# Kernel optimization log

Hardware: AMD Instinct MI355X
Metric: run time of the kernel (lower is better)

## Reference

```python
import jax, jax.numpy as jnp
import numpy as np

FORE_TH = 0.5
BACK_TH = 0.4
MAX_FOR_TARGET = True
FOREGROUND_ONLY = False  # return both foreground and background masks


def _cxcywh_to_xyxy(b):
    cx, cy, w, h = b[..., 0], b[..., 1], b[..., 2], b[..., 3]
    return jnp.stack([cx - w * 0.5, cy - h * 0.5, cx + w * 0.5, cy + h * 0.5], axis=-1)


def _batch_iou(anchors_xyxy, boxes_xyxy):
    # anchors_xyxy: [A,4], boxes_xyxy: [B,T,4] -> ious [B,A,T]
    a = anchors_xyxy[None, :, None, :]   # [1,A,1,4]
    b = boxes_xyxy[:, None, :, :]        # [B,1,T,4]
    lt = jnp.maximum(a[..., :2], b[..., :2])
    rb = jnp.minimum(a[..., 2:], b[..., 2:])
    wh = jnp.clip(rb - lt, 0.0)
    inter = wh[..., 0] * wh[..., 1]                                   # [B,A,T]
    area_a = (a[..., 2] - a[..., 0]) * (a[..., 3] - a[..., 1])
    area_b = (b[..., 2] - b[..., 0]) * (b[..., 3] - b[..., 1])
    return inter / (area_a + area_b - inter + 1e-9)


def setup_inputs() -> dict:
    key = jax.random.key(0)
    k1, k2 = jax.random.split(key)
    labels = jax.random.uniform(k1, (8, 64, 84), dtype=jnp.float32)
    anchors = jax.random.uniform(k2, (1, 100000, 4), dtype=jnp.float32)
    return {"labels": labels, "anchors": anchors}


def reference(labels, anchors):
    # labels: [B, T, 4+C] (cxcywh + class), anchors: [1, A, 4] (cxcywh)
    B = labels.shape[0]
    a_xyxy = _cxcywh_to_xyxy(anchors[0])           # [A,4]
    b_xyxy = _cxcywh_to_xyxy(labels[..., :4])      # [B,T,4]
    ious = _batch_iou(a_xyxy, b_xyxy)              # [B,A,T]

    max_iou_anchor = jnp.max(ious, axis=2)         # [B,A] best IoU per anchor
    target_for_anchor = jnp.argmax(ious, axis=2)   # [B,A] best target per anchor

    fore_mask = max_iou_anchor >= FORE_TH          # [B,A]
    if MAX_FOR_TARGET:
        anchor_for_target = jnp.argmax(ious, axis=1)        # [B,T] best anchor per target
        batch_idx = jnp.arange(B)[:, None]
        fm_t = jnp.zeros(fore_mask.shape, dtype=bool).at[batch_idx, anchor_for_target].set(True)
        fore_mask = jnp.logical_or(fore_mask, fm_t)

    back_mask = jnp.logical_not(fore_mask)
    if BACK_TH is not None:
        back_mask = jnp.logical_and(back_mask, max_iou_anchor < BACK_TH)

    # label[target_for_anchor] per batch -> [B, A, 4+C]
    assigned_target = jnp.take_along_axis(labels, target_for_anchor[..., None], axis=1)

    # Fixed-shape equivalent of the original list-of-dicts with nonzero():
    # (foreground mask, background mask, per-anchor assigned labels).
    return fore_mask, back_mask, assigned_target
```

## Files before the change

kernel.cpp:

```cpp
#include <hip/hip_runtime.h>
#include <stdint.h>

typedef unsigned long long u64;

#define N_ANCH 100000
#define BATCH 8
#define NTGT 64
#define NFEAT 84
#define BLK 256
#define NWAVE (BLK / 64)
#define NBX ((N_ANCH + BLK - 1) / BLK)
#define GCHUNK (NFEAT / 4)

template <bool FULL>
__device__ __forceinline__ void iou_loop(
    const int tid, const int wave, const int n, const bool valid,
    const float4* __restrict__ tbox, const float* __restrict__ sarea,
    u64* __restrict__ board, const float* __restrict__ anchors, u64& bestA)
{
#pragma clang fp contract(off)
    const int nld = FULL ? n : (valid ? n : 0);
    const float4 ab = *(const float4*)(anchors + (size_t)nld * 4);
    const float ax1 = ab.x - ab.z * 0.5f;
    const float ay1 = ab.y - ab.w * 0.5f;
    const float ax2 = ab.x + ab.z * 0.5f;
    const float ay2 = ab.y + ab.w * 0.5f;
    const float areaA = (ax2 - ax1) * (ay2 - ay1);
    const u64 pn = (u64)(0xFFFFFFFFu - (uint32_t)n);

    for (int s = 0; s < NTGT; ++s) {
        const int t = (tid + s) & (NTGT - 1);
        const float4 tb = tbox[t];
        const float areaB = sarea[t];

        const float w = fmaxf(fminf(ax2, tb.z) - fmaxf(ax1, tb.x), 0.0f);
        const float h = fmaxf(fminf(ay2, tb.w) - fmaxf(ay1, tb.y), 0.0f);
        const float inter = w * h;
        const float iou = inter / (((areaA + areaB) - inter) + 1e-9f);
        const uint32_t ib = __float_as_uint(iou);

        const u64 pa = ((u64)ib << 32) | (u64)(63 - t);
        bestA = pa > bestA ? pa : bestA;

        u64 c = ((u64)ib << 32) | pn;
        if (!FULL) c = valid ? c : 0ull;
        atomicMax(&board[(size_t)wave * NTGT + t], c);
    }
}

__global__ __launch_bounds__(BLK) void fused_kernel(
    const float* __restrict__ labels,
    const float* __restrict__ anchors,
    float* __restrict__ out_fore,
    float* __restrict__ out_back,
    float* __restrict__ out_assigned,
    u64* __restrict__ ws_part)
{
#pragma clang fp contract(off)
    __shared__ float4 tbox[NTGT];
    __shared__ float sarea[NTGT];
    __shared__ u64 board[NWAVE * NTGT];
    __shared__ int sidx[BLK];

    const int b    = blockIdx.y;
    const int bx   = blockIdx.x;
    const int tid  = threadIdx.x;
    const int wave = tid >> 6;

    if (tid < NTGT) {
        const float4 box = *(const float4*)(labels + ((size_t)b * NTGT + tid) * NFEAT);
        const float x1 = box.x - box.z * 0.5f;
        const float y1 = box.y - box.w * 0.5f;
        const float x2 = box.x + box.z * 0.5f;
        const float y2 = box.y + box.w * 0.5f;
        tbox[tid] = make_float4(x1, y1, x2, y2);
        sarea[tid] = (x2 - x1) * (y2 - y1);
    }
    board[tid] = 0ull;
    __syncthreads();

    const int n = bx * BLK + tid;
    u64 bestA = 0ull;
    bool valid = true;
    if (bx != NBX - 1) {
        iou_loop<true>(tid, wave, n, true, tbox, sarea, board, anchors, bestA);
    } else {
        valid = (n < N_ANCH);
        iou_loop<false>(tid, wave, n, valid, tbox, sarea, board, anchors, bestA);
    }

    if (valid) {
        const float mi = __uint_as_float((uint32_t)(bestA >> 32));
        const int   bt = 63 - (int)(bestA & 0xFFFFFFFFull);
        const bool fore = (mi >= 0.5f);
        const bool back = (!fore) && (mi < 0.4f);
        const size_t o = (size_t)b * N_ANCH + n;
        out_fore[o] = fore ? 1.0f : 0.0f;
        out_back[o] = back ? 1.0f : 0.0f;
        sidx[tid] = bt;
    } else {
        sidx[tid] = 0;
    }
    __syncthreads();

    if (tid < NTGT) {
        const u64 m0 = board[tid];
        const u64 m1 = board[NTGT + tid];
        const u64 m2 = board[2 * NTGT + tid];
        const u64 m3 = board[3 * NTGT + tid];
        const u64 a = m0 > m1 ? m0 : m1;
        const u64 c = m2 > m3 ? m2 : m3;
        ws_part[((size_t)b * NTGT + tid) * NBX + bx] = a > c ? a : c;
    }

    const float* lab_b = labels + (size_t)b * NTGT * NFEAT;
    float* out_b = out_assigned + ((size_t)b * N_ANCH + (size_t)bx * BLK) * NFEAT;
    for (int i = tid; i < BLK * GCHUNK; i += BLK) {
        const int nl = i / GCHUNK;
        const int k  = i - nl * GCHUNK;
        if (bx * BLK + nl < N_ANCH) {
            const int t = sidx[nl];
            const float4 v = *(const float4*)(lab_b + (size_t)t * NFEAT + k * 4);
            *(float4*)(out_b + (size_t)nl * NFEAT + (size_t)k * 4) = v;
        }
    }
}

__global__ __launch_bounds__(64) void fixup_kernel(
    const u64* __restrict__ ws_part,
    float* __restrict__ out_fore,
    float* __restrict__ out_back)
{
    const int bt   = blockIdx.x;
    const int lane = threadIdx.x;
    const u64* p = ws_part + (size_t)bt * NBX;

    u64 best = 0ull;
    for (int i = lane; i < NBX; i += 64) {
        const u64 v = p[i];
        best = v > best ? v : best;
    }
    for (int off = 32; off > 0; off >>= 1) {
        const u64 o = __shfl_down(best, off, 64);
        best = o > best ? o : best;
    }
    if (lane == 0) {
        const uint32_t n = 0xFFFFFFFFu - (uint32_t)(best & 0xFFFFFFFFull);
        const int b = bt >> 6;
        const size_t o = (size_t)b * N_ANCH + n;
        out_fore[o] = 1.0f;
        out_back[o] = 0.0f;
    }
}

extern "C" void kernel_launch(void* const* d_in, const int* in_sizes, int n_in,
                              void* d_out, int out_size, void* d_ws, size_t ws_size,
                              hipStream_t stream) {
    const float* labels  = (const float*)d_in[0];
    const float* anchors = (const float*)d_in[1];

    float* out_fore     = (float*)d_out;
    float* out_back     = out_fore + (size_t)BATCH * N_ANCH;
    float* out_assigned = out_back + (size_t)BATCH * N_ANCH;

    u64* ws_part = (u64*)d_ws;

    dim3 gridA(NBX, BATCH);
    fused_kernel<<<gridA, BLK, 0, stream>>>(labels, anchors, out_fore, out_back,
                                            out_assigned, ws_part);

    fixup_kernel<<<BATCH * NTGT, 64, 0, stream>>>(ws_part, out_fore, out_back);
}
```

Before: 291.1 us.

## Split label gather out of IoU kernel into separate flat gather kernel

Moves the per-anchor label gather out of the fused IoU kernel. The IoU kernel now writes the best-target index to a workspace array, and a new fully parallel kernel copies the labels using a flat float4 index. This is meant to spread the large output write, about 269 MB, across many more threads instead of tying it to the compute-bound IoU blocks. In exchange it adds a kernel launch and an extra round trip of target indices through global memory.

```diff
diff --git a/kernel.cpp b/kernel.cpp
--- a/kernel.cpp
+++ b/kernel.cpp
@@ -11,6 +11,7 @@
 #define NWAVE (BLK / 64)
 #define NBX ((N_ANCH + BLK - 1) / BLK)
 #define GCHUNK (NFEAT / 4)
+#define CPB (N_ANCH * GCHUNK)
 
 template <bool FULL>
 __device__ __forceinline__ void iou_loop(
@@ -48,19 +49,18 @@
     }
 }
 
-__global__ __launch_bounds__(BLK) void fused_kernel(
+__global__ __launch_bounds__(BLK) void loop_kernel(
     const float* __restrict__ labels,
     const float* __restrict__ anchors,
     float* __restrict__ out_fore,
     float* __restrict__ out_back,
-    float* __restrict__ out_assigned,
+    int* __restrict__ ws_tgt,
     u64* __restrict__ ws_part)
 {
 #pragma clang fp contract(off)
     __shared__ float4 tbox[NTGT];
     __shared__ float sarea[NTGT];
     __shared__ u64 board[NWAVE * NTGT];
-    __shared__ int sidx[BLK];
 
     const int b    = blockIdx.y;
     const int bx   = blockIdx.x;
@@ -97,9 +97,7 @@
         const size_t o = (size_t)b * N_ANCH + n;
         out_fore[o] = fore ? 1.0f : 0.0f;
         out_back[o] = back ? 1.0f : 0.0f;
-        sidx[tid] = bt;
-    } else {
-        sidx[tid] = 0;
+        ws_tgt[o] = bt;
     }
     __syncthreads();
 
@@ -111,18 +109,6 @@
         const u64 a = m0 > m1 ? m0 : m1;
         const u64 c = m2 > m3 ? m2 : m3;
         ws_part[((size_t)b * NTGT + tid) * NBX + bx] = a > c ? a : c;
-    }
-
-    const float* lab_b = labels + (size_t)b * NTGT * NFEAT;
-    float* out_b = out_assigned + ((size_t)b * N_ANCH + (size_t)bx * BLK) * NFEAT;
-    for (int i = tid; i < BLK * GCHUNK; i += BLK) {
-        const int nl = i / GCHUNK;
-        const int k  = i - nl * GCHUNK;
-        if (bx * BLK + nl < N_ANCH) {
-            const int t = sidx[nl];
-            const float4 v = *(const float4*)(lab_b + (size_t)t * NFEAT + k * 4);
-            *(float4*)(out_b + (size_t)nl * NFEAT + (size_t)k * 4) = v;
-        }
     }
 }
 
@@ -153,6 +139,23 @@
     }
 }
 
+__global__ __launch_bounds__(BLK) void gather_kernel(
+    const float* __restrict__ labels,
+    const int* __restrict__ ws_tgt,
+    float* __restrict__ out_assigned)
+{
+    const int b = blockIdx.y;
+    const unsigned int c = blockIdx.x * BLK + threadIdx.x;
+    if (c < CPB) {
+        const unsigned int n = c / 21u;
+        const unsigned int k = c - n * 21u;
+        const int t = ws_tgt[(size_t)b * N_ANCH + n];
+        const float4 v = *(const float4*)(labels + ((size_t)b * NTGT + t) * NFEAT
+                                          + (size_t)k * 4);
+        *(float4*)(out_assigned + (size_t)b * (N_ANCH * NFEAT) + (size_t)c * 4) = v;
+    }
+}
+
 extern "C" void kernel_launch(void* const* d_in, const int* in_sizes, int n_in,
                               void* d_out, int out_size, void* d_ws, size_t ws_size,
                               hipStream_t stream) {
@@ -164,10 +167,14 @@
     float* out_assigned = out_back + (size_t)BATCH * N_ANCH;
 
     u64* ws_part = (u64*)d_ws;
+    int* ws_tgt  = (int*)((char*)d_ws + (size_t)BATCH * NTGT * NBX * sizeof(u64));
 
     dim3 gridA(NBX, BATCH);
-    fused_kernel<<<gridA, BLK, 0, stream>>>(labels, anchors, out_fore, out_back,
-                                            out_assigned, ws_part);
+    loop_kernel<<<gridA, BLK, 0, stream>>>(labels, anchors, out_fore, out_back,
+                                           ws_tgt, ws_part);
 
     fixup_kernel<<<BATCH * NTGT, 64, 0, stream>>>(ws_part, out_fore, out_back);
+
+    dim3 gridC((CPB + BLK - 1) / BLK, BATCH);
+    gather_kernel<<<gridC, BLK, 0, stream>>>(labels, ws_tgt, out_assigned);
 }
```

New measurement: 320.3 us. 1.1x slower.
